# Performance work log

Measured on AMD Instinct MI355X. Metric: run time of the kernel, lower is better.

## Reference

```python
import jax, jax.numpy as jnp
import numpy as np

B, L, K, D = 1, 4096, 24, 512


def setup_inputs() -> dict:
    key = jax.random.key(0)
    k1, k2, k3, k4 = jax.random.split(key, 4)
    u = jax.random.normal(k1, (B, L, D), dtype=jnp.float32)
    # spectral filter bank (learned parameter initialized from Hankel eigenvectors in the
    # original; random init is equivalent for a correctness baseline), scaled ~O(1/sqrt(L))
    filters = jax.random.normal(k2, (L, K), dtype=jnp.float32) * (1.0 / np.sqrt(L))
    M_phi_plus = jax.random.normal(k3, (K, D, D), dtype=jnp.float32) * (1.0 / np.sqrt(K * D))
    M_phi_minus = jax.random.normal(k4, (K, D, D), dtype=jnp.float32) * (1.0 / np.sqrt(K * D))
    return {"u": u, "filters": filters, "M_phi_plus": M_phi_plus, "M_phi_minus": M_phi_minus}


def _causal_conv(u, phi):
    # Causal linear convolution of every input channel with every spectral filter via FFT.
    # u: [B, L, D], phi: [L, K] -> [B, L, K, D]
    L_ = u.shape[1]
    n = 2 * L_  # zero-pad so circular FFT conv == linear causal conv
    Uf = jnp.fft.rfft(u, n=n, axis=1)                    # [B, F, D]
    Pf = jnp.fft.rfft(phi, n=n, axis=0)                  # [F, K]
    prod = Uf[:, :, None, :] * Pf[None, :, :, None]      # [B, F, K, D]
    return jnp.fft.irfft(prod, n=n, axis=1)[:, :L_]      # [B, L, K, D]


def reference(u, filters, M_phi_plus, M_phi_minus):
    L_ = u.shape[1]
    # sgn[t] = (-1)^t ; U_minus[b,l,k,d] = sum_s u[b,s,d] * phi[l-s,k] * (-1)^(l-s),
    # which equals convolving with the alternating-sign filter phi[t]*(-1)^t
    # (the original implements this as sgn-pre/post-multiplication around FlashFFTConv).
    sgn = jnp.where(jnp.arange(L_) % 2 == 0, 1.0, -1.0).astype(u.dtype)
    U_plus = _causal_conv(u, filters)                      # [B, L, K, D]
    U_minus = _causal_conv(u, filters * sgn[:, None])      # [B, L, K, D]
    y = (jnp.einsum('blkd,kdo->blo', U_plus, M_phi_plus)
         + jnp.einsum('blkd,kdo->blo', U_minus, M_phi_minus))
    return y
```

## Files before the change

kernel.cpp:

```cpp
#include <hip/hip_runtime.h>
#include <hip/hip_bf16.h>
#include <cstdint>
#include <cstddef>

using bf16 = __hip_bfloat16;

typedef __attribute__((ext_vector_type(4))) float f32x4;
typedef __attribute__((ext_vector_type(8))) short s16x8;

#define LSEQ 4096
#define DDIM 512
#define KFLT 24
#define NFFT 8192
#define MR 8192

__device__ __forceinline__ void gld16(const bf16* g, bf16* l) {
  __builtin_amdgcn_global_load_lds((const __attribute__((address_space(1))) void*)g,
                                   (__attribute__((address_space(3))) void*)l, 16, 0, 0);
}

#define MEMFENCE asm volatile("" ::: "memory")
#define BAR() do { MEMFENCE; __builtin_amdgcn_s_barrier(); MEMFENCE; } while (0)

__device__ __forceinline__ float fsin_rev(float rev) {
  float s; asm("v_sin_f32 %0, %1" : "=v"(s) : "v"(rev)); return s;
}
__device__ __forceinline__ float fcos_rev(float rev) {
  float c; asm("v_cos_f32 %0, %1" : "=v"(c) : "v"(rev)); return c;
}

__device__ __forceinline__ void stage_half(const bf16* g, int ldk, bf16* ldsbase,
                                           int wave, int lane) {
  const int r8 = lane >> 3;
  const int sc = ((lane & 7) ^ r8) * 8;
  #pragma unroll
  for (int q = 0; q < 2; ++q) {
    const int c = wave * 2 + q;
    gld16(g + (size_t)(c * 8 + r8) * ldk + sc, ldsbase + c * 512);
  }
}

__device__ __forceinline__ s16x8 ldfrag(const bf16* buf, int row, int kk, int l4) {
  return *(const s16x8*)(buf + row * 64 + (((kk * 4 + l4) ^ (row & 7)) * 8));
}

__global__ __launch_bounds__(256) void transpose_cast(
    const float* __restrict__ in, bf16* __restrict__ out, int R, int C) {
  __shared__ float tile[32][33];
  const size_t bo = (size_t)blockIdx.z * R * C;
  const float* inb = in + bo;
  bf16* outb = out + bo;
  int c0 = blockIdx.x * 32, r0 = blockIdx.y * 32;
  int tx = threadIdx.x & 31, ty = threadIdx.x >> 5;
  #pragma unroll
  for (int i = 0; i < 32; i += 8)
    tile[ty + i][tx] = inb[(size_t)(r0 + ty + i) * C + (c0 + tx)];
  __syncthreads();
  #pragma unroll
  for (int i = 0; i < 32; i += 8)
    outb[(size_t)(c0 + ty + i) * R + (r0 + tx)] = __float2bfloat16(tile[tx][ty + i]);
}

__global__ __launch_bounds__(256) void add2_cast(
    const bf16* __restrict__ P, bf16* __restrict__ out) {
  size_t i = ((size_t)blockIdx.x * 256 + threadIdx.x) * 8;
  const size_t MN = (size_t)MR * DDIM;
  s16x8 a = *(const s16x8*)(P + i);
  s16x8 b = *(const s16x8*)(P + i + MN);
  bf16 o[8];
  #pragma unroll
  for (int e = 0; e < 8; ++e) {
    float fa = __uint_as_float((unsigned)(unsigned short)a[e] << 16);
    float fb = __uint_as_float((unsigned)(unsigned short)b[e] << 16);
    o[e] = __float2bfloat16(fa + fb);
  }
  *(s16x8*)(out + i) = *(const s16x8*)o;
}

__global__ __launch_bounds__(256) void tr_reduce4(
    const float* __restrict__ S, bf16* __restrict__ out) {
  __shared__ float tile[32][33];
  int c0 = blockIdx.x * 32, r0 = blockIdx.y * 32;
  int tx = threadIdx.x & 31, ty = threadIdx.x >> 5;
  const int nt = c0 >> 8;
  const int scl = (c0 & 255) + tx;
  const size_t SB = (size_t)MR * 256;
  #pragma unroll
  for (int i = 0; i < 32; i += 8) {
    size_t ro = (size_t)(r0 + ty + i) * 256 + scl;
    tile[ty + i][tx] = S[(0 * 2 + nt) * SB + ro] + S[(1 * 2 + nt) * SB + ro] +
                       S[(2 * 2 + nt) * SB + ro] + S[(3 * 2 + nt) * SB + ro];
  }
  __syncthreads();
  #pragma unroll
  for (int i = 0; i < 32; i += 8)
    out[(size_t)(c0 + ty + i) * MR + (r0 + tx)] = __float2bfloat16(tile[tx][ty + i]);
}

__global__ __launch_bounds__(256) void reduce4y(
    const float* __restrict__ P, const float* __restrict__ vnyq,
    float* __restrict__ y) {
  size_t i = ((size_t)blockIdx.x * 256 + threadIdx.x) * 4;
  const size_t MN = (size_t)LSEQ * DDIM;
  int l = (int)(i >> 9), o = (int)(i & 511);
  f32x4 a = *(const f32x4*)(P + i);
  f32x4 b = *(const f32x4*)(P + i + MN);
  f32x4 c = *(const f32x4*)(P + i + 2 * MN);
  f32x4 d = *(const f32x4*)(P + i + 3 * MN);
  f32x4 v = *(const f32x4*)(vnyq + o);
  float sg = (l & 1) ? -(1.f / NFFT) : (1.f / NFFT);
  f32x4 r = a + b + c + d;
  r[0] += sg * v[0]; r[1] += sg * v[1]; r[2] += sg * v[2]; r[3] += sg * v[3];
  *(f32x4*)(y + i) = r;
}

__global__ __launch_bounds__(256) void gen_w(bf16* __restrict__ W) {
  int r = blockIdx.y;
  int t0 = (blockIdx.x * 256 + threadIdx.x) * 8;
  int f = r >> 1;
  bool odd = r & 1;
  bf16 o[8];
  #pragma unroll
  for (int i = 0; i < 8; ++i) {
    int m = (f * (t0 + i)) & (NFFT - 1);
    float rev = (float)m * (1.f / NFFT);
    float v = odd ? -fsin_rev(rev) : fcos_rev(rev);
    o[i] = __float2bfloat16(v);
  }
  *(s16x8*)(W + (size_t)r * LSEQ + t0) = *(const s16x8*)o;
}

__global__ __launch_bounds__(256) void gen_cinv(bf16* __restrict__ Cinv) {
  int l = blockIdx.y;
  int r0 = (blockIdx.x * 256 + threadIdx.x) * 8;
  bf16 o[8];
  #pragma unroll
  for (int p = 0; p < 4; ++p) {
    int f = (r0 >> 1) + p;
    int m = (f * l) & (NFFT - 1);
    float rev = (float)m * (1.f / NFFT);
    float sc = ((f == 0) ? 1.f : 2.f) * (1.f / NFFT);
    o[2 * p] = __float2bfloat16(sc * fcos_rev(rev));
    o[2 * p + 1] = __float2bfloat16(-sc * fsin_rev(rev));
  }
  *(s16x8*)(Cinv + (size_t)l * MR + r0) = *(const s16x8*)o;
}

__global__ __launch_bounds__(256) void compute_pf(
    const float* __restrict__ phi, float* __restrict__ Pf) {
  int f0 = blockIdx.x * 2;
  int tid = threadIdx.x;
  int lane = tid & 63, wave = tid >> 6;
  float pre[2][KFLT], pim[2][KFLT];
  #pragma unroll
  for (int ff = 0; ff < 2; ++ff)
    #pragma unroll
    for (int k = 0; k < KFLT; ++k) { pre[ff][k] = 0.f; pim[ff][k] = 0.f; }
  for (int cch = 0; cch < LSEQ / 256; ++cch) {
    int t = cch * 256 + tid;
    const float4* pv = (const float4*)(phi + (size_t)t * KFLT);
    float4 v0 = pv[0], v1 = pv[1], v2 = pv[2], v3 = pv[3], v4 = pv[4], v5 = pv[5];
    float pr[KFLT] = {v0.x, v0.y, v0.z, v0.w, v1.x, v1.y, v1.z, v1.w,
                      v2.x, v2.y, v2.z, v2.w, v3.x, v3.y, v3.z, v3.w,
                      v4.x, v4.y, v4.z, v4.w, v5.x, v5.y, v5.z, v5.w};
    #pragma unroll
    for (int ff = 0; ff < 2; ++ff) {
      int m = ((f0 + ff) * t) & (NFFT - 1);
      float rev = (float)m * (1.f / NFFT);
      float s = fsin_rev(rev), c = fcos_rev(rev);
      #pragma unroll
      for (int k = 0; k < KFLT; ++k) {
        pre[ff][k] += pr[k] * c;
        pim[ff][k] -= pr[k] * s;
      }
    }
  }
  __shared__ float red[4][2][2 * KFLT];
  #pragma unroll
  for (int ff = 0; ff < 2; ++ff)
    #pragma unroll
    for (int k = 0; k < KFLT; ++k) {
      float r = pre[ff][k], i2 = pim[ff][k];
      #pragma unroll
      for (int off = 32; off > 0; off >>= 1) {
        r += __shfl_down(r, off, 64);
        i2 += __shfl_down(i2, off, 64);
      }
      if (lane == 0) { red[wave][ff][2 * k] = r; red[wave][ff][2 * k + 1] = i2; }
    }
  __syncthreads();
  if (tid < 96) {
    int ff = tid / 48, q = tid % 48;
    int f = f0 + ff;
    if (f <= NFFT / 2)
      Pf[(size_t)f * 48 + q] =
          red[0][ff][q] + red[1][ff][q] + red[2][ff][q] + red[3][ff][q];
  }
}

__global__ __launch_bounds__(256) void build_pw(
    const float* __restrict__ Pf, float* __restrict__ Pw, float* __restrict__ wnyq) {
  int idx = blockIdx.x * 256 + threadIdx.x;
  int j = idx >> 12, f = idx & 4095;
  float re, im;
  if (j < KFLT) {
    re = Pf[(size_t)f * 48 + j * 2];
    im = Pf[(size_t)f * 48 + j * 2 + 1];
  } else {
    int k = j - KFLT, g = NFFT / 2 - f;
    re = Pf[(size_t)g * 48 + k * 2];
    im = -Pf[(size_t)g * 48 + k * 2 + 1];
  }
  Pw[(size_t)idx * 2] = re;
  Pw[(size_t)idx * 2 + 1] = im;
  if (idx < 48)
    wnyq[idx] = (idx < KFLT) ? Pf[(size_t)(NFFT / 2) * 48 + idx * 2]
                             : Pf[(idx - KFLT) * 2];
}

__global__ __launch_bounds__(256) void nyq_u(
    const float* __restrict__ u, float* __restrict__ Unyq) {
  int d = blockIdx.x * 256 + threadIdx.x;
  int t0 = blockIdx.y * 64;
  float acc = 0.f;
  for (int t = t0; t < t0 + 64; t += 2)
    acc += u[(size_t)t * DDIM + d] - u[(size_t)(t + 1) * DDIM + d];
  atomicAdd(&Unyq[d], acc);
}

__global__ __launch_bounds__(256) void vnyq_k(
    const bf16* __restrict__ Mt, const float* __restrict__ Unyq,
    const float* __restrict__ wnyq, float* __restrict__ vnyq) {
  __shared__ float us[DDIM];
  int j = blockIdx.x, tid = threadIdx.x;
  us[tid] = Unyq[tid];
  us[tid + 256] = Unyq[tid + 256];
  __syncthreads();
  float w = wnyq[j];
  int o = blockIdx.y * 128 + (tid >> 1);
  int dh = (tid & 1) * 256;
  const bf16* row = Mt + ((size_t)j * DDIM + o) * DDIM + dh;
  float acc = 0.f;
  for (int d0 = 0; d0 < 256; d0 += 8) {
    s16x8 v = *(const s16x8*)(row + d0);
    #pragma unroll
    for (int e = 0; e < 8; ++e)
      acc += us[dh + d0 + e] * __uint_as_float((unsigned)(unsigned short)v[e] << 16);
  }
  acc += __shfl_xor(acc, 1, 64);
  if ((tid & 1) == 0) atomicAdd(&vnyq[o], w * acc);
}

template <int STORE>
__global__ __launch_bounds__(512, 2) void gemmD(
    const bf16* __restrict__ A, const bf16* __restrict__ Bt, int ldk,
    bf16* __restrict__ Obf, float* __restrict__ Of) {
  __shared__ bf16 sA[3 * 128 * 64];
  __shared__ bf16 sB[3 * 256 * 64];

  const int lin = blockIdx.x;
  const int wid = (lin & 7) * 32 + (lin >> 3);

  int mt, nt, kt0, nkt, ks;
  if constexpr (STORE == 0) {
    ks = wid >> 7; int rem = wid & 127; mt = rem >> 1; nt = rem & 1;
    kt0 = ks * 32; nkt = 32;
  } else {
    ks = wid >> 6; int rem = wid & 63; mt = rem >> 1; nt = rem & 1;
    kt0 = ks * 32; nkt = 32;
  }

  const int tid = threadIdx.x, lane = tid & 63, wave = tid >> 6;
  const int l15 = lane & 15, l4 = lane >> 4;
  const int wr = wave >> 2, wc = wave & 3;
  const int mtile = mt * 128, ntile = nt * 256;
  const bf16* Ab = A + (size_t)mtile * ldk;
  const bf16* Bb = Bt + (size_t)ntile * ldk;

  f32x4 acc[4][4];
  #pragma unroll
  for (int m = 0; m < 4; ++m)
    #pragma unroll
    for (int n = 0; n < 4; ++n) acc[m][n] = f32x4{0.f, 0.f, 0.f, 0.f};

  auto stage = [&](int t, int buf) {
    const size_t ko = (size_t)(kt0 + t) * 64;
    stage_half(Ab + ko, ldk, sA + buf * (128 * 64), wave, lane);
    stage_half(Bb + ko, ldk, sB + buf * (256 * 64), wave, lane);
    stage_half(Bb + (size_t)128 * ldk + ko, ldk, sB + buf * (256 * 64) + 128 * 64,
               wave, lane);
  };

  stage(0, 0);
  stage(1, 1);
  asm volatile("s_waitcnt vmcnt(6)" ::: "memory");
  BAR();

  for (int t = 0; t < nkt; ++t) {
    const int buf = t % 3;
    const bf16* bA = sA + buf * (128 * 64);
    const bf16* bB = sB + buf * (256 * 64);
    const bool i2 = (t + 2 < nkt);

    s16x8 afr[4][2], bfr[4][2];
    #pragma unroll
    for (int n = 0; n < 4; ++n)
      #pragma unroll
      for (int kk = 0; kk < 2; ++kk)
        bfr[n][kk] = ldfrag(bB, wc * 64 + n * 16 + l15, kk, l4);
    #pragma unroll
    for (int m = 0; m < 4; ++m)
      #pragma unroll
      for (int kk = 0; kk < 2; ++kk)
        afr[m][kk] = ldfrag(bA, wr * 64 + m * 16 + l15, kk, l4);

    if (i2) stage(t + 2, (t + 2) % 3);

    __builtin_amdgcn_s_setprio(1);
    #pragma unroll
    for (int m = 0; m < 4; ++m)
      #pragma unroll
      for (int n = 0; n < 4; ++n)
        #pragma unroll
        for (int kk = 0; kk < 2; ++kk)
          acc[m][n] = __builtin_amdgcn_mfma_f32_16x16x32_bf16(
              afr[m][kk], bfr[n][kk], acc[m][n], 0, 0, 0);
    __builtin_amdgcn_s_setprio(0);

    if (i2) { asm volatile("s_waitcnt vmcnt(6)" ::: "memory"); }
    else    { asm volatile("s_waitcnt vmcnt(0)" ::: "memory"); }
    BAR();
  }

  #pragma unroll
  for (int m = 0; m < 4; ++m)
    #pragma unroll
    for (int n = 0; n < 4; ++n)
      #pragma unroll
      for (int e = 0; e < 4; ++e) {
        int row = mtile + wr * 64 + m * 16 + l4 * 4 + e;
        int col = ntile + wc * 64 + n * 16 + l15;
        if constexpr (STORE == 0)
          Obf[(size_t)ks * MR * DDIM + (size_t)row * DDIM + col] =
              __float2bfloat16(acc[m][n][e]);
        else
          Of[(size_t)ks * LSEQ * DDIM + (size_t)row * DDIM + col] = acc[m][n][e];
      }
}

struct ARegs { int4 a[4]; float2 w[2]; };

__global__ __launch_bounds__(512, 2) void gemmW(
    const bf16* __restrict__ Auf, const bf16* __restrict__ Mt,
    const float* __restrict__ Pw, float* __restrict__ Slots) {
  __shared__ bf16 sA[2 * 256 * 64];
  __shared__ bf16 sB[3 * 256 * 64];

  const int lin = blockIdx.x;
  const int q = lin & 7;
  const int pos = lin >> 3;
  const int jg = q >> 1, mhalf = q & 1;
  const int nt = pos >> 4;
  const int mt = mhalf * 16 + (pos & 15);

  const int tid = threadIdx.x, lane = tid & 63, wave = tid >> 6;
  const int l15 = lane & 15, l4 = lane >> 4;
  const int wr = wave >> 2, wc = wave & 3;
  const int r8 = lane >> 3, c8 = lane & 7;

  float* dst = Slots + (size_t)(jg * 2 + nt) * ((size_t)MR * 256);

  f32x4 acc[8][4];
  #pragma unroll
  for (int m = 0; m < 8; ++m)
    #pragma unroll
    for (int n = 0; n < 4; ++n) acc[m][n] = f32x4{0.f, 0.f, 0.f, 0.f};

  auto J  = [&](int s) { return jg * 12 + (s >> 3); };
  auto KT = [&](int s) { return s & 7; };

  auto issueA = [&](int j, int kt, ARegs& r) {
    #pragma unroll
    for (int qq = 0; qq < 2; ++qq) {
      int row_e = wave * 32 + 2 * (qq * 8 + r8);
      int rg = mt * 256 + row_e;
      const bf16* p = Auf + (size_t)rg * DDIM + kt * 64 + c8 * 8;
      r.a[2 * qq]     = *(const int4*)p;
      r.a[2 * qq + 1] = *(const int4*)(p + DDIM);
      r.w[qq] = *(const float2*)(Pw + ((size_t)j * 4096 + (rg >> 1)) * 2);
    }
  };
  auto writeA = [&](bf16* db, const ARegs& r) {
    #pragma unroll
    for (int qq = 0; qq < 2; ++qq) {
      int row_e = wave * 32 + 2 * (qq * 8 + r8);
      union { int4 i; unsigned short u[8]; } ae, ao;
      ae.i = r.a[2 * qq]; ao.i = r.a[2 * qq + 1];
      bf16 oe[8], oo[8];
      #pragma unroll
      for (int e = 0; e < 8; ++e) {
        float fe = __uint_as_float((unsigned)ae.u[e] << 16);
        float fo = __uint_as_float((unsigned)ao.u[e] << 16);
        oe[e] = __float2bfloat16(r.w[qq].x * fe - r.w[qq].y * fo);
        oo[e] = __float2bfloat16(r.w[qq].x * fo + r.w[qq].y * fe);
      }
      *(s16x8*)(db + row_e * 64 + ((c8 ^ (row_e & 7)) * 8)) = *(const s16x8*)oe;
      *(s16x8*)(db + (row_e + 1) * 64 + ((c8 ^ ((row_e + 1) & 7)) * 8)) =
          *(const s16x8*)oo;
    }
  };
  auto stageB = [&](int j, int kt, bf16* db) {
    const bf16* bb = Mt + (size_t)j * (DDIM * DDIM) + (size_t)(nt * 256) * DDIM + kt * 64;
    stage_half(bb, DDIM, db, wave, lane);
    stage_half(bb + (size_t)128 * DDIM, DDIM, db + 128 * 64, wave, lane);
  };

  ARegs rA, rB_;

  {
    ARegs t0;
    issueA(J(0), KT(0), t0);
    stageB(J(0), KT(0), sB);
    asm volatile("s_waitcnt vmcnt(4)" ::: "memory");
    writeA(sA, t0);
    issueA(J(1), KT(1), rA);
    stageB(J(1), KT(1), sB + 256 * 64);
    asm volatile("s_waitcnt vmcnt(10)" ::: "memory");
    asm volatile("s_waitcnt lgkmcnt(0)" ::: "memory");
    BAR();
  }

  auto unit = [&](int s, ARegs& cur, ARegs& nxt) {
    const bf16* bA = sA + (s & 1) * (256 * 64);
    const bf16* bB = sB + (s % 3) * (256 * 64);
    const bool i2 = (s + 2 < 96);

    s16x8 bfr[4][2], afr[4][2];
    #pragma unroll
    for (int n = 0; n < 4; ++n)
      #pragma unroll
      for (int kk = 0; kk < 2; ++kk)
        bfr[n][kk] = ldfrag(bB, wc * 64 + n * 16 + l15, kk, l4);
    #pragma unroll
    for (int m = 0; m < 4; ++m)
      #pragma unroll
      for (int kk = 0; kk < 2; ++kk)
        afr[m][kk] = ldfrag(bA, wr * 128 + m * 16 + l15, kk, l4);

    if (i2) {
      issueA(J(s + 2), KT(s + 2), nxt);
      stageB(J(s + 2), KT(s + 2), sB + ((s + 2) % 3) * (256 * 64));
    }

    __builtin_amdgcn_s_setprio(1);
    #pragma unroll
    for (int m = 0; m < 4; ++m)
      #pragma unroll
      for (int n = 0; n < 4; ++n)
        #pragma unroll
        for (int kk = 0; kk < 2; ++kk)
          acc[m][n] = __builtin_amdgcn_mfma_f32_16x16x32_bf16(
              afr[m][kk], bfr[n][kk], acc[m][n], 0, 0, 0);
    __builtin_amdgcn_s_setprio(0);

    #pragma unroll
    for (int m = 0; m < 4; ++m)
      #pragma unroll
      for (int kk = 0; kk < 2; ++kk)
        afr[m][kk] = ldfrag(bA, wr * 128 + 64 + m * 16 + l15, kk, l4);

    if (s + 1 < 96) {
      if (i2) { asm volatile("s_waitcnt vmcnt(10)" ::: "memory"); }
      else    { asm volatile("s_waitcnt vmcnt(0)" ::: "memory"); }
      writeA(sA + ((s + 1) & 1) * (256 * 64), cur);
    }

    __builtin_amdgcn_s_setprio(1);
    #pragma unroll
    for (int m = 0; m < 4; ++m)
      #pragma unroll
      for (int n = 0; n < 4; ++n)
        #pragma unroll
        for (int kk = 0; kk < 2; ++kk)
          acc[4 + m][n] = __builtin_amdgcn_mfma_f32_16x16x32_bf16(
              afr[m][kk], bfr[n][kk], acc[4 + m][n], 0, 0, 0);
    __builtin_amdgcn_s_setprio(0);

    asm volatile("s_waitcnt lgkmcnt(0)" ::: "memory");
    BAR();
  };

  for (int sp = 0; sp < 48; ++sp) {
    unit(2 * sp,     rA, rB_);
    unit(2 * sp + 1, rB_, rA);
  }

  #pragma unroll
  for (int m = 0; m < 8; ++m)
    #pragma unroll
    for (int n = 0; n < 4; ++n)
      #pragma unroll
      for (int e = 0; e < 4; ++e) {
        int row = mt * 256 + wr * 128 + (m & 3) * 16 + (m >> 2) * 64 + l4 * 4 + e;
        int col = wc * 64 + n * 16 + l15;
        dst[(size_t)row * 256 + col] = acc[m][n][e];
      }
}

#define WS_W     0ULL
#define WS_AUF   67108864ULL
#define WS_UT    75497472ULL
#define WS_MT    79691776ULL
#define WS_PF    104857600ULL
#define WS_PW    105644288ULL
#define WS_WNYQ  107217152ULL
#define WS_UNYQ  107217408ULL
#define WS_VNYQ  107219456ULL
#define WS_YBT   107221504ULL
#define WS_G1P   115610112ULL
#define WS_TOTAL 132387328ULL

extern "C" void kernel_launch(void* const* d_in, const int* in_sizes, int n_in,
                              void* d_out, int out_size, void* d_ws, size_t ws_size,
                              hipStream_t stream) {
  const float* u   = (const float*)d_in[0];
  const float* phi = (const float*)d_in[1];
  const float* Mp  = (const float*)d_in[2];
  const float* Mm  = (const float*)d_in[3];
  float* y = (float*)d_out;

  if (ws_size < WS_TOTAL) return;

  char* ws = (char*)d_ws;
  bf16*  W    = (bf16*)(ws + WS_W);
  float* Slots= (float*)(ws + WS_W);
  bf16*  Auf  = (bf16*)(ws + WS_AUF);
  bf16*  uT   = (bf16*)(ws + WS_UT);
  bf16*  Mt   = (bf16*)(ws + WS_MT);
  float* Pf   = (float*)(ws + WS_PF);
  float* Pw   = (float*)(ws + WS_PW);
  float* wny  = (float*)(ws + WS_WNYQ);
  float* Uny  = (float*)(ws + WS_UNYQ);
  float* vny  = (float*)(ws + WS_VNYQ);
  bf16*  Ybt  = (bf16*)(ws + WS_YBT);
  bf16*  G1P  = (bf16*)(ws + WS_G1P);
  float* G3P  = (float*)(ws + WS_AUF);

  transpose_cast<<<dim3(16, 128, 1), 256, 0, stream>>>(u, uT, LSEQ, DDIM);
  transpose_cast<<<dim3(16, 16, 24), 256, 0, stream>>>(Mp, Mt, DDIM, DDIM);
  transpose_cast<<<dim3(16, 16, 24), 256, 0, stream>>>(Mm, Mt + (size_t)24 * DDIM * DDIM,
                                                       DDIM, DDIM);
  gen_w<<<dim3(2, MR), 256, 0, stream>>>(W);
  compute_pf<<<dim3(2049), 256, 0, stream>>>(phi, Pf);
  build_pw<<<dim3(48 * 4096 / 256), 256, 0, stream>>>(Pf, Pw, wny);
  hipMemsetAsync(Uny, 0, DDIM * sizeof(float), stream);
  nyq_u<<<dim3(2, 64), 256, 0, stream>>>(u, Uny);

  gemmD<0><<<256, 512, 0, stream>>>(W, uT, LSEQ, G1P, nullptr);
  add2_cast<<<dim3(MR * DDIM / 2048), 256, 0, stream>>>(G1P, Auf);

  gemmW<<<256, 512, 0, stream>>>(Auf, Mt, Pw, Slots);

  tr_reduce4<<<dim3(16, 256), 256, 0, stream>>>(Slots, Ybt);
  hipMemsetAsync(vny, 0, DDIM * sizeof(float), stream);
  vnyq_k<<<dim3(48, 4), 256, 0, stream>>>(Mt, Uny, wny, vny);

  gen_cinv<<<dim3(4, LSEQ), 256, 0, stream>>>(W);
  gemmD<1><<<256, 512, 0, stream>>>(W, Ybt, MR, nullptr, G3P);
  reduce4y<<<dim3(LSEQ * DDIM / 1024), 256, 0, stream>>>(G3P, vny, y);
}
```

Baseline: 502.5 us.

## Generate DFT twiddle tiles on the fly inside GEMMs instead of materializing matrices

Removes the gen_w and gen_cinv kernels that wrote the bf16 forward and inverse DFT matrices (tens of MB) to global memory. The GEMMs now compute the A-operand twiddle factors directly into LDS each k-step, using the same swizzled layout stage_half produced. This drops the matrix writes, the re-reads and two launches. In exchange it adds trig ALU work and LDS stores inside the pipelined main loop, plus an lgkmcnt wait before each barrier.

```diff
diff --git a/kernel.cpp b/kernel.cpp
--- a/kernel.cpp
+++ b/kernel.cpp
@@ -114,38 +114,6 @@
   *(f32x4*)(y + i) = r;
 }
 
-__global__ __launch_bounds__(256) void gen_w(bf16* __restrict__ W) {
-  int r = blockIdx.y;
-  int t0 = (blockIdx.x * 256 + threadIdx.x) * 8;
-  int f = r >> 1;
-  bool odd = r & 1;
-  bf16 o[8];
-  #pragma unroll
-  for (int i = 0; i < 8; ++i) {
-    int m = (f * (t0 + i)) & (NFFT - 1);
-    float rev = (float)m * (1.f / NFFT);
-    float v = odd ? -fsin_rev(rev) : fcos_rev(rev);
-    o[i] = __float2bfloat16(v);
-  }
-  *(s16x8*)(W + (size_t)r * LSEQ + t0) = *(const s16x8*)o;
-}
-
-__global__ __launch_bounds__(256) void gen_cinv(bf16* __restrict__ Cinv) {
-  int l = blockIdx.y;
-  int r0 = (blockIdx.x * 256 + threadIdx.x) * 8;
-  bf16 o[8];
-  #pragma unroll
-  for (int p = 0; p < 4; ++p) {
-    int f = (r0 >> 1) + p;
-    int m = (f * l) & (NFFT - 1);
-    float rev = (float)m * (1.f / NFFT);
-    float sc = ((f == 0) ? 1.f : 2.f) * (1.f / NFFT);
-    o[2 * p] = __float2bfloat16(sc * fcos_rev(rev));
-    o[2 * p + 1] = __float2bfloat16(-sc * fsin_rev(rev));
-  }
-  *(s16x8*)(Cinv + (size_t)l * MR + r0) = *(const s16x8*)o;
-}
-
 __global__ __launch_bounds__(256) void compute_pf(
     const float* __restrict__ phi, float* __restrict__ Pf) {
   int f0 = blockIdx.x * 2;
@@ -252,8 +220,8 @@
 }
 
 template <int STORE>
-__global__ __launch_bounds__(512, 2) void gemmD(
-    const bf16* __restrict__ A, const bf16* __restrict__ Bt, int ldk,
+__global__ __launch_bounds__(512, 2) void gemmG(
+    const bf16* __restrict__ Bt, int ldk,
     bf16* __restrict__ Obf, float* __restrict__ Of) {
   __shared__ bf16 sA[3 * 128 * 64];
   __shared__ bf16 sB[3 * 256 * 64];
@@ -273,8 +241,8 @@
   const int tid = threadIdx.x, lane = tid & 63, wave = tid >> 6;
   const int l15 = lane & 15, l4 = lane >> 4;
   const int wr = wave >> 2, wc = wave & 3;
+  const int r8 = lane >> 3, c8 = lane & 7;
   const int mtile = mt * 128, ntile = nt * 256;
-  const bf16* Ab = A + (size_t)mtile * ldk;
   const bf16* Bb = Bt + (size_t)ntile * ldk;
 
   f32x4 acc[4][4];
@@ -283,17 +251,51 @@
     #pragma unroll
     for (int n = 0; n < 4; ++n) acc[m][n] = f32x4{0.f, 0.f, 0.f, 0.f};
 
-  auto stage = [&](int t, int buf) {
+  auto genA = [&](int t, int buf) {
+    const int kbase = (kt0 + t) * 64 + ((c8 ^ r8) * 8);
+    #pragma unroll
+    for (int q = 0; q < 2; ++q) {
+      const int c = wave * 2 + q;
+      const int row = mtile + c * 8 + r8;
+      bf16 o[8];
+      if constexpr (STORE == 0) {
+        const int f = row >> 1;
+        const bool odd = row & 1;
+        #pragma unroll
+        for (int e = 0; e < 8; ++e) {
+          int m = (f * (kbase + e)) & (NFFT - 1);
+          float rev = (float)m * (1.f / NFFT);
+          o[e] = __float2bfloat16(odd ? -fsin_rev(rev) : fcos_rev(rev));
+        }
+      } else {
+        #pragma unroll
+        for (int e = 0; e < 8; ++e) {
+          int r = kbase + e;
+          int f = r >> 1;
+          int m = (f * row) & (NFFT - 1);
+          float rev = (float)m * (1.f / NFFT);
+          float sc2 = ((f == 0) ? 1.f : 2.f) * (1.f / NFFT);
+          o[e] = __float2bfloat16((r & 1) ? -sc2 * fsin_rev(rev)
+                                          : sc2 * fcos_rev(rev));
+        }
+      }
+      *(s16x8*)(sA + buf * (128 * 64) + (c * 8 + r8) * 64 + c8 * 8) =
+          *(const s16x8*)o;
+    }
+  };
+  auto stageB = [&](int t, int buf) {
     const size_t ko = (size_t)(kt0 + t) * 64;
-    stage_half(Ab + ko, ldk, sA + buf * (128 * 64), wave, lane);
     stage_half(Bb + ko, ldk, sB + buf * (256 * 64), wave, lane);
     stage_half(Bb + (size_t)128 * ldk + ko, ldk, sB + buf * (256 * 64) + 128 * 64,
                wave, lane);
   };
 
-  stage(0, 0);
-  stage(1, 1);
-  asm volatile("s_waitcnt vmcnt(6)" ::: "memory");
+  genA(0, 0);
+  genA(1, 1);
+  stageB(0, 0);
+  stageB(1, 1);
+  asm volatile("s_waitcnt vmcnt(4)" ::: "memory");
+  asm volatile("s_waitcnt lgkmcnt(0)" ::: "memory");
   BAR();
 
   for (int t = 0; t < nkt; ++t) {
@@ -314,7 +316,10 @@
       for (int kk = 0; kk < 2; ++kk)
         afr[m][kk] = ldfrag(bA, wr * 64 + m * 16 + l15, kk, l4);
 
-    if (i2) stage(t + 2, (t + 2) % 3);
+    if (i2) {
+      genA(t + 2, (t + 2) % 3);
+      stageB(t + 2, (t + 2) % 3);
+    }
 
     __builtin_amdgcn_s_setprio(1);
     #pragma unroll
@@ -327,8 +332,9 @@
               afr[m][kk], bfr[n][kk], acc[m][n], 0, 0, 0);
     __builtin_amdgcn_s_setprio(0);
 
-    if (i2) { asm volatile("s_waitcnt vmcnt(6)" ::: "memory"); }
+    if (i2) { asm volatile("s_waitcnt vmcnt(4)" ::: "memory"); }
     else    { asm volatile("s_waitcnt vmcnt(0)" ::: "memory"); }
+    asm volatile("s_waitcnt lgkmcnt(0)" ::: "memory");
     BAR();
   }
 
@@ -532,7 +538,6 @@
   if (ws_size < WS_TOTAL) return;
 
   char* ws = (char*)d_ws;
-  bf16*  W    = (bf16*)(ws + WS_W);
   float* Slots= (float*)(ws + WS_W);
   bf16*  Auf  = (bf16*)(ws + WS_AUF);
   bf16*  uT   = (bf16*)(ws + WS_UT);
@@ -550,13 +555,12 @@
   transpose_cast<<<dim3(16, 16, 24), 256, 0, stream>>>(Mp, Mt, DDIM, DDIM);
   transpose_cast<<<dim3(16, 16, 24), 256, 0, stream>>>(Mm, Mt + (size_t)24 * DDIM * DDIM,
                                                        DDIM, DDIM);
-  gen_w<<<dim3(2, MR), 256, 0, stream>>>(W);
   compute_pf<<<dim3(2049), 256, 0, stream>>>(phi, Pf);
   build_pw<<<dim3(48 * 4096 / 256), 256, 0, stream>>>(Pf, Pw, wny);
   hipMemsetAsync(Uny, 0, DDIM * sizeof(float), stream);
   nyq_u<<<dim3(2, 64), 256, 0, stream>>>(u, Uny);
 
-  gemmD<0><<<256, 512, 0, stream>>>(W, uT, LSEQ, G1P, nullptr);
+  gemmG<0><<<256, 512, 0, stream>>>(uT, LSEQ, G1P, nullptr);
   add2_cast<<<dim3(MR * DDIM / 2048), 256, 0, stream>>>(G1P, Auf);
 
   gemmW<<<256, 512, 0, stream>>>(Auf, Mt, Pw, Slots);
@@ -565,7 +569,6 @@
   hipMemsetAsync(vny, 0, DDIM * sizeof(float), stream);
   vnyq_k<<<dim3(48, 4), 256, 0, stream>>>(Mt, Uny, wny, vny);
 
-  gen_cinv<<<dim3(4, LSEQ), 256, 0, stream>>>(W);
-  gemmD<1><<<256, 512, 0, stream>>>(W, Ybt, MR, nullptr, G3P);
+  gemmG<1><<<256, 512, 0, stream>>>(Ybt, MR, nullptr, G3P);
   reduce4y<<<dim3(LSEQ * DDIM / 1024), 256, 0, stream>>>(G3P, vny, y);
 }
```

After: 488.8 us. 2.7% less time.
